# Kernel optimization log

Hardware: AMD Instinct MI355X
Metric: run time of the kernel (lower is better)

The kernel has to match this reference:

```python
import jax, jax.numpy as jnp
import numpy as np

# Config mirrors init_kwargs
D_IN, D_OUT, HEADS, SEQ, BATCH = 1024, 64, 16, 2048, 2


def setup_inputs() -> dict:
    key = jax.random.key(0)
    kx, kq, kk, kv = jax.random.split(key, 4)
    scale = 1.0 / np.sqrt(D_IN)
    x = jax.random.normal(kx, (BATCH, SEQ, D_IN), dtype=jnp.float32)
    # Stacked per-head projection weights, [H, d_in, d_out] (qkv_bias=False)
    Wq = jax.random.normal(kq, (HEADS, D_IN, D_OUT), dtype=jnp.float32) * scale
    Wk = jax.random.normal(kk, (HEADS, D_IN, D_OUT), dtype=jnp.float32) * scale
    Wv = jax.random.normal(kv, (HEADS, D_IN, D_OUT), dtype=jnp.float32) * scale
    return {"x": x, "Wq": Wq, "Wk": Wk, "Wv": Wv}


def reference(x, Wq, Wk, Wv):
    # x: [B, S, d_in]; W*: [H, d_in, d_out]
    q = jnp.einsum("bsd,hde->bhse", x, Wq)
    k = jnp.einsum("bsd,hde->bhse", x, Wk)
    v = jnp.einsum("bsd,hde->bhse", x, Wv)
    scores = jnp.einsum("bhse,bhte->bhst", q, k) / jnp.sqrt(
        jnp.asarray(D_OUT, dtype=q.dtype)
    )
    S = x.shape[1]
    causal = jnp.tril(jnp.ones((S, S), dtype=bool))  # [S, S]
    scores = jnp.where(causal[None, None], scores, -jnp.inf)
    attn = jax.nn.softmax(scores, axis=-1)  # dropout=0.0 (eval)
    ctx = jnp.einsum("bhst,bhte->bhse", attn, v)  # [B, H, S, d_out]
    # concat heads on last dim -> [B, S, H*d_out]
    B, H, S2, E = ctx.shape
    return jnp.transpose(ctx, (0, 2, 1, 3)).reshape(B, S2, H * E)
```

## Files before the change

kernel.cpp:

```cpp
#include <hip/hip_runtime.h>
#include <hip/hip_bf16.h>
#include <math.h>

#define BATCH 2
#define SEQ   2048
#define DIN   1024
#define HEADS 16
#define EDIM  64

#define NX   (BATCH*SEQ*DIN)
#define NW   (3*HEADS*DIN*EDIM)
#define NQKV (BATCH*HEADS*SEQ*EDIM)

#define QSCALE 0.18033688011112042f

typedef __attribute__((ext_vector_type(8))) short short8;
typedef __attribute__((ext_vector_type(4))) float f32x4;

static __device__ __forceinline__ ushort f2bf(float f) {
    __hip_bfloat16 h = __float2bfloat16(f);
    return *reinterpret_cast<ushort*>(&h);
}

static __device__ __forceinline__ void gload16(const void* g, void* l) {
    void* gv = const_cast<void*>(g);
    __builtin_amdgcn_global_load_lds(
        (__attribute__((address_space(1))) void*)gv,
        (__attribute__((address_space(3))) void*)l,
        16, 0, 0);
}

__global__ __launch_bounds__(256) void prep(
    const float* __restrict__ x, const float* __restrict__ Wq,
    const float* __restrict__ Wk, const float* __restrict__ Wv,
    ushort* __restrict__ xb, ushort* __restrict__ wt)
{
    const int t = threadIdx.x;
    if (blockIdx.x < 1024) {
        const int v0 = blockIdx.x * 256 + t;
#pragma unroll
        for (int i = 0; i < 4; ++i) {
            int i4 = (v0 + i * 262144) * 4;
            float4 f = *(const float4*)(x + i4);
            ushort4 o;
            o.x = f2bf(f.x); o.y = f2bf(f.y); o.z = f2bf(f.z); o.w = f2bf(f.w);
            *(ushort4*)(xb + i4) = o;
        }
    } else {
        const int bid = blockIdx.x - 1024;
        const int dt  = bid & 15;
        const int h   = (bid >> 4) & 15;
        const int mat = bid >> 8;

        const float* W = (mat == 0) ? Wq : (mat == 1) ? Wk : Wv;
        const float* src = W + ((size_t)h * DIN + dt * 64) * EDIM;
        ushort* dst = wt + ((size_t)(mat * HEADS + h) * EDIM) * DIN + dt * 64;

        __shared__ ushort T[64][68];
#pragma unroll
        for (int i = 0; i < 16; ++i) {
            int v = t + i * 256;
            int d = v >> 6, e = v & 63;
            T[d][e] = f2bf(src[(size_t)d * EDIM + e]);
        }
        __syncthreads();
#pragma unroll
        for (int i = 0; i < 4; ++i) {
            int v = t + i * 256;
            int e = v >> 4, d4 = (v & 15) << 2;
            ushort4 ov;
            ov.x = T[d4 + 0][e]; ov.y = T[d4 + 1][e];
            ov.z = T[d4 + 2][e]; ov.w = T[d4 + 3][e];
            *(ushort4*)&dst[(size_t)e * DIN + d4] = ov;
        }
    }
}

__global__ __launch_bounds__(256) void qkv_gemm(
    const ushort* __restrict__ xb, const ushort* __restrict__ wt,
    ushort* __restrict__ qkv)
{
    const int bid = blockIdx.x;
    const int xcd = bid & 7;
    const int idx = bid >> 3;
    const int mt  = (xcd >> 1) * 8 + idx / 12;
    const int nt  = (xcd & 1) * 12 + idx % 12;
    const int m0 = mt * 128, n0 = nt * 128;
    const int b  = mt >> 4;

    __shared__ ushort As[2][128][64];
    __shared__ ushort Bs[2][128][64];

    const int t    = threadIdx.x;
    const int lane = t & 63;
    const int w    = t >> 6;
    const int wr   = w >> 1, wc = w & 1;
    const int fr   = lane & 15;
    const int fk   = (lane >> 4) * 8;
    const int rg   = (lane >> 4) * 4;
    const int sw   = (fr & 7) << 3;

    const ushort* xbase = xb + (size_t)m0 * DIN;
    const ushort* wbase = wt + (size_t)n0 * DIN;

    const int lrow = lane >> 3;
    const int lcol = ((lane & 7) ^ (lane >> 3)) << 3;

    f32x4 acc[4][4];
#pragma unroll
    for (int i = 0; i < 4; ++i)
#pragma unroll
        for (int j = 0; j < 4; ++j) acc[i][j] = (f32x4)0.f;

#pragma unroll
    for (int j = 0; j < 4; ++j) {
        const int c = w * 4 + j;
        gload16(&xbase[(size_t)(c * 8 + lrow) * DIN + lcol], &As[0][c * 8][0]);
        gload16(&wbase[(size_t)(c * 8 + lrow) * DIN + lcol], &Bs[0][c * 8][0]);
    }
    __syncthreads();

    for (int kt = 0; kt < DIN / 64; ++kt) {
        const int cur = kt & 1;

        if (kt + 1 < DIN / 64) {
            const int k0 = (kt + 1) * 64;
            const int nxt = cur ^ 1;
#pragma unroll
            for (int j = 0; j < 4; ++j) {
                const int c = w * 4 + j;
                gload16(&xbase[(size_t)(c * 8 + lrow) * DIN + k0 + lcol], &As[nxt][c * 8][0]);
                gload16(&wbase[(size_t)(c * 8 + lrow) * DIN + k0 + lcol], &Bs[nxt][c * 8][0]);
            }
        }

        short8 a[4][2], bfr[4][2];
#pragma unroll
        for (int rb = 0; rb < 4; ++rb)
#pragma unroll
            for (int kk = 0; kk < 2; ++kk) {
                a[rb][kk]   = *(const short8*)&As[cur][wr * 64 + rb * 16 + fr][(kk * 32 + fk) ^ sw];
                bfr[rb][kk] = *(const short8*)&Bs[cur][wc * 64 + rb * 16 + fr][(kk * 32 + fk) ^ sw];
            }
#pragma unroll
        for (int kk = 0; kk < 2; ++kk)
#pragma unroll
            for (int rb = 0; rb < 4; ++rb)
#pragma unroll
                for (int cf = 0; cf < 4; ++cf)
                    acc[rb][cf] = __builtin_amdgcn_mfma_f32_16x16x32_bf16(a[rb][kk], bfr[cf][kk], acc[rb][cf], 0, 0, 0);

        __syncthreads();
    }

    const int hg  = nt * 2 + wc;
    const int mat = hg >> 4;
    const int h   = hg & 15;
    const int s0  = (m0 & 2047) + wr * 64;
    if (mat < 2) {
        const float sc = (mat == 0) ? QSCALE : 1.0f;
        ushort* dst = qkv + (size_t)mat * NQKV
                    + ((size_t)((b * HEADS + h) * SEQ) + s0) * EDIM;
#pragma unroll
        for (int rb = 0; rb < 4; ++rb)
#pragma unroll
            for (int cf = 0; cf < 4; ++cf)
#pragma unroll
                for (int i = 0; i < 4; ++i)
                    dst[(size_t)(rb * 16 + rg + i) * EDIM + cf * 16 + fr] = f2bf(acc[rb][cf][i] * sc);
    } else {
        ushort* vtb = qkv + (size_t)2 * NQKV + ((size_t)(b * HEADS + h) * EDIM) * SEQ;
#pragma unroll
        for (int rb = 0; rb < 4; ++rb)
#pragma unroll
            for (int cf = 0; cf < 4; ++cf) {
                ushort4 ov;
                ov.x = f2bf(acc[rb][cf][0]); ov.y = f2bf(acc[rb][cf][1]);
                ov.z = f2bf(acc[rb][cf][2]); ov.w = f2bf(acc[rb][cf][3]);
                *(ushort4*)&vtb[(size_t)(cf * 16 + fr) * SEQ + s0 + rb * 16 + rg] = ov;
            }
    }
}

__global__ __launch_bounds__(512) void flash_mfma(
    const ushort* __restrict__ q, const ushort* __restrict__ k,
    const ushort* __restrict__ vt, float* __restrict__ out)
{
    const int bid = blockIdx.x;
    const int it  = 15 - (bid >> 5);
    const int bh  = bid & 31;
    const int b   = bh >> 4;
    const int h   = bh & 15;
    const int KT  = 2 * it + 2;

    const ushort* Qb  = q  + ((size_t)((b * HEADS + h) * SEQ) + it * 128) * EDIM;
    const ushort* Kb  = k  + ((size_t)((b * HEADS + h) * SEQ)) * EDIM;
    const ushort* Vtb = vt + ((size_t)((b * HEADS + h) * EDIM)) * SEQ;

    __shared__ ushort Ks_[2][64][72];
    __shared__ ushort Vs_[2][64][72];
    __shared__ ushort Ps_[8][16][72];

    const int t    = threadIdx.x;
    const int lane = t & 63;
    const int w    = t >> 6;
    const int fr   = lane & 15;
    const int fk   = (lane >> 4) * 8;
    const int rg   = (lane >> 4) * 4;

    const int srow = t >> 3;
    const int scol = (t & 7) * 8;

    const int wrow0 = it * 128 + w * 16;
    const int lastT = wrow0 >> 6;
    const int qrow  = wrow0 + fr;

    short8 qf[2];
#pragma unroll
    for (int kk = 0; kk < 2; ++kk)
        qf[kk] = *(const short8*)&Qb[(size_t)(w * 16 + fr) * EDIM + kk * 32 + fk];

    f32x4 o_[4];
#pragma unroll
    for (int cf = 0; cf < 4; ++cf) o_[cf] = (f32x4)0.f;
    float lpart = 0.f;

    uint4 krv = *(const uint4*)&Kb[(size_t)srow * EDIM + scol];
    uint4 vrv = *(const uint4*)&Vtb[(size_t)srow * SEQ + scol];
    *(uint4*)&Ks_[0][srow][scol] = krv;
    *(uint4*)&Vs_[0][srow][scol] = vrv;
    __syncthreads();

    for (int kt = 0; kt < KT; ++kt) {
        const int cur = kt & 1;

        if (kt + 1 < KT) {
            krv = *(const uint4*)&Kb[(size_t)((kt + 1) * 64 + srow) * EDIM + scol];
            vrv = *(const uint4*)&Vtb[(size_t)srow * SEQ + (kt + 1) * 64 + scol];
        }

        if (kt <= lastT) {
            f32x4 s[4];
#pragma unroll
            for (int cf = 0; cf < 4; ++cf) s[cf] = (f32x4)0.f;
#pragma unroll
            for (int cf = 0; cf < 4; ++cf)
#pragma unroll
                for (int kk = 0; kk < 2; ++kk) {
                    short8 kf = *(const short8*)&Ks_[cur][cf * 16 + fr][kk * 32 + fk];
                    s[cf] = __builtin_amdgcn_mfma_f32_16x16x32_bf16(kf, qf[kk], s[cf], 0, 0, 0);
                }

            const bool dm = (kt == lastT);
            if (dm) {
#pragma unroll
                for (int cf = 0; cf < 4; ++cf)
#pragma unroll
                    for (int i = 0; i < 4; ++i) {
                        int kpos = kt * 64 + cf * 16 + rg + i;
                        if (kpos > qrow) s[cf][i] = -1e30f;
                    }
            }

            float ls = 0.f;
#pragma unroll
            for (int cf = 0; cf < 4; ++cf) {
                float p0 = __builtin_amdgcn_exp2f(s[cf][0]);
                float p1 = __builtin_amdgcn_exp2f(s[cf][1]);
                float p2 = __builtin_amdgcn_exp2f(s[cf][2]);
                float p3 = __builtin_amdgcn_exp2f(s[cf][3]);
                ls += (p0 + p1) + (p2 + p3);
                uint2 pk;
                pk.x = (uint)f2bf(p0) | ((uint)f2bf(p1) << 16);
                pk.y = (uint)f2bf(p2) | ((uint)f2bf(p3) << 16);
                *(uint2*)&Ps_[w][fr][cf * 16 + rg] = pk;
            }
            lpart += ls;

            short8 pf[2];
#pragma unroll
            for (int kb = 0; kb < 2; ++kb)
                pf[kb] = *(const short8*)&Ps_[w][fr][kb * 32 + fk];
#pragma unroll
            for (int cf = 0; cf < 4; ++cf)
#pragma unroll
                for (int kb = 0; kb < 2; ++kb) {
                    short8 vf = *(const short8*)&Vs_[cur][cf * 16 + fr][kb * 32 + fk];
                    o_[cf] = __builtin_amdgcn_mfma_f32_16x16x32_bf16(vf, pf[kb], o_[cf], 0, 0, 0);
                }
        }

        if (kt + 1 < KT) {
            const int nxt = cur ^ 1;
            *(uint4*)&Ks_[nxt][srow][scol] = krv;
            *(uint4*)&Vs_[nxt][srow][scol] = vrv;
            __syncthreads();
        }
    }

    float ls = lpart;
    ls += __shfl_xor(ls, 16);
    ls += __shfl_xor(ls, 32);
    const float inv = 1.f / ls;

    float* rowp = out + ((size_t)(b * SEQ + qrow)) * (HEADS * EDIM) + h * EDIM;
#pragma unroll
    for (int cf = 0; cf < 4; ++cf) {
        f32x4 ov = o_[cf] * inv;
        *(f32x4*)&rowp[cf * 16 + rg] = ov;
    }
}

extern "C" void kernel_launch(void* const* d_in, const int* in_sizes, int n_in,
                              void* d_out, int out_size, void* d_ws, size_t ws_size,
                              hipStream_t stream) {
    const float* x  = (const float*)d_in[0];
    const float* Wq = (const float*)d_in[1];
    const float* Wk = (const float*)d_in[2];
    const float* Wv = (const float*)d_in[3];
    float* out = (float*)d_out;

    ushort* xb  = (ushort*)d_ws;
    ushort* wt  = xb + NX;
    ushort* qkv = wt + NW;

    prep<<<1792, 256, 0, stream>>>(x, Wq, Wk, Wv, xb, wt);
    qkv_gemm<<<768, 256, 0, stream>>>(xb, wt, qkv);
    flash_mfma<<<BATCH * HEADS * (SEQ / 128), 512, 0, stream>>>(
        qkv, qkv + NQKV, qkv + (size_t)2 * NQKV, out);
}
```

Baseline: 93.52 us.

## Pipeline QKV projection GEMM with two-stage prefetch and explicit waitcnt barriers

Restructures the QKV projection GEMM main loop so two k-tiles are in flight. Each iteration waits only on the older tile with vmcnt(8), loads fragments into registers, then barriers before reusing the same LDS buffer for the tile two steps ahead. MFMAs are issued after the next global-to-LDS loads. The goal is to hide global load latency behind compute and replace __syncthreads with finer-grained waits. The cost is manual waitcnt correctness and an extra barrier per iteration.

```diff
diff --git a/kernel.cpp b/kernel.cpp
--- a/kernel.cpp
+++ b/kernel.cpp
@@ -28,6 +28,12 @@
         (__attribute__((address_space(1))) void*)gv,
         (__attribute__((address_space(3))) void*)l,
         16, 0, 0);
+}
+
+static __device__ __forceinline__ void barrier_fenced() {
+    asm volatile("" ::: "memory");
+    __builtin_amdgcn_s_barrier();
+    asm volatile("" ::: "memory");
 }
 
 __global__ __launch_bounds__(256) void prep(
@@ -106,52 +112,76 @@
     const int lrow = lane >> 3;
     const int lcol = ((lane & 7) ^ (lane >> 3)) << 3;
 
+#define STAGE(buf, k0)                                                          \
+    {                                                                           \
+        _Pragma("unroll")                                                       \
+        for (int j = 0; j < 4; ++j) {                                           \
+            const int c = w * 4 + j;                                            \
+            gload16(&xbase[(size_t)(c * 8 + lrow) * DIN + (k0) + lcol], &As[buf][c * 8][0]); \
+            gload16(&wbase[(size_t)(c * 8 + lrow) * DIN + (k0) + lcol], &Bs[buf][c * 8][0]); \
+        }                                                                       \
+    }
+
     f32x4 acc[4][4];
 #pragma unroll
     for (int i = 0; i < 4; ++i)
 #pragma unroll
         for (int j = 0; j < 4; ++j) acc[i][j] = (f32x4)0.f;
 
-#pragma unroll
-    for (int j = 0; j < 4; ++j) {
-        const int c = w * 4 + j;
-        gload16(&xbase[(size_t)(c * 8 + lrow) * DIN + lcol], &As[0][c * 8][0]);
-        gload16(&wbase[(size_t)(c * 8 + lrow) * DIN + lcol], &Bs[0][c * 8][0]);
-    }
-    __syncthreads();
-
-    for (int kt = 0; kt < DIN / 64; ++kt) {
+    STAGE(0, 0);
+    STAGE(1, 64);
+
+    short8 a[4][2], bfr[4][2];
+
+#define LOAD_FRAGS(cur)                                                         \
+    {                                                                           \
+        _Pragma("unroll")                                                       \
+        for (int rb = 0; rb < 4; ++rb)                                          \
+            _Pragma("unroll")                                                   \
+            for (int kk = 0; kk < 2; ++kk) {                                    \
+                a[rb][kk]   = *(const short8*)&As[cur][wr * 64 + rb * 16 + fr][(kk * 32 + fk) ^ sw]; \
+                bfr[rb][kk] = *(const short8*)&Bs[cur][wc * 64 + rb * 16 + fr][(kk * 32 + fk) ^ sw]; \
+            }                                                                   \
+    }
+
+#define DO_MFMA()                                                               \
+    {                                                                           \
+        _Pragma("unroll")                                                       \
+        for (int kk = 0; kk < 2; ++kk)                                          \
+            _Pragma("unroll")                                                   \
+            for (int rb = 0; rb < 4; ++rb)                                      \
+                _Pragma("unroll")                                               \
+                for (int cf = 0; cf < 4; ++cf)                                  \
+                    acc[rb][cf] = __builtin_amdgcn_mfma_f32_16x16x32_bf16(a[rb][kk], bfr[cf][kk], acc[rb][cf], 0, 0, 0); \
+    }
+
+    for (int kt = 0; kt < 15; ++kt) {
         const int cur = kt & 1;
 
-        if (kt + 1 < DIN / 64) {
-            const int k0 = (kt + 1) * 64;
-            const int nxt = cur ^ 1;
-#pragma unroll
-            for (int j = 0; j < 4; ++j) {
-                const int c = w * 4 + j;
-                gload16(&xbase[(size_t)(c * 8 + lrow) * DIN + k0 + lcol], &As[nxt][c * 8][0]);
-                gload16(&wbase[(size_t)(c * 8 + lrow) * DIN + k0 + lcol], &Bs[nxt][c * 8][0]);
-            }
-        }
-
-        short8 a[4][2], bfr[4][2];
-#pragma unroll
-        for (int rb = 0; rb < 4; ++rb)
-#pragma unroll
-            for (int kk = 0; kk < 2; ++kk) {
-                a[rb][kk]   = *(const short8*)&As[cur][wr * 64 + rb * 16 + fr][(kk * 32 + fk) ^ sw];
-                bfr[rb][kk] = *(const short8*)&Bs[cur][wc * 64 + rb * 16 + fr][(kk * 32 + fk) ^ sw];
-            }
-#pragma unroll
-        for (int kk = 0; kk < 2; ++kk)
-#pragma unroll
-            for (int rb = 0; rb < 4; ++rb)
-#pragma unroll
-                for (int cf = 0; cf < 4; ++cf)
-                    acc[rb][cf] = __builtin_amdgcn_mfma_f32_16x16x32_bf16(a[rb][kk], bfr[cf][kk], acc[rb][cf], 0, 0, 0);
-
-        __syncthreads();
-    }
+        asm volatile("s_waitcnt vmcnt(8)" ::: "memory");
+        __builtin_amdgcn_sched_barrier(0);
+        barrier_fenced();
+
+        LOAD_FRAGS(cur);
+
+        asm volatile("s_waitcnt lgkmcnt(0)" ::: "memory");
+        __builtin_amdgcn_sched_barrier(0);
+        barrier_fenced();
+
+        if (kt <= 13) STAGE(cur, (kt + 2) * 64);
+
+        DO_MFMA();
+    }
+    {
+        asm volatile("s_waitcnt vmcnt(0)" ::: "memory");
+        __builtin_amdgcn_sched_barrier(0);
+        barrier_fenced();
+        LOAD_FRAGS(1);
+        DO_MFMA();
+    }
+#undef STAGE
+#undef LOAD_FRAGS
+#undef DO_MFMA
 
     const int hg  = nt * 2 + wc;
     const int mat = hg >> 4;
```

Measured after the change: 85.28 us. 1.1x faster.
